# Performance work log

Measured on AMD Instinct MI355X. Metric: run time of the kernel, lower is better.

The kernel has to match this reference:

```python
import jax, jax.numpy as jnp
import numpy as np

N, C, E = 32768, 256, 16
LN_EPS = 1e-5
ENT_EPS = 1e-12


def setup_inputs() -> dict:
    key = jax.random.key(0)
    ks = jax.random.split(key, 8)
    return {
        "inputs": jax.random.normal(ks[0], (N, C), jnp.float32),
        "conv_out": jax.random.normal(ks[1], (N, C), jnp.float32),
        "domain_emb": jax.random.normal(ks[2], (C,), jnp.float32),
        "share_W": jax.random.normal(ks[3], (C, C), jnp.float32) * 0.02,
        "share_b": jnp.zeros((C,), jnp.float32),
        "gate_W": jax.random.normal(ks[4], (C, E), jnp.float32) * 0.1,
        "gate_b": jnp.zeros((E,), jnp.float32),
        "expert_W": jax.random.normal(ks[5], (E, C, C), jnp.float32) * 0.02,
        "expert_b": jnp.zeros((E, C), jnp.float32),
        "ln_gamma": jnp.ones((C,), jnp.float32),
        "ln_beta": jnp.zeros((C,), jnp.float32),
    }


def reference(inputs, conv_out, domain_emb, share_W, share_b, gate_W, gate_b,
              expert_W, expert_b, ln_gamma, ln_beta):
    n_exp = gate_W.shape[-1]

    # shared expert
    share_out = inputs @ share_W + share_b                      # (N, C)

    # LayerNorm on (stand-in) sparse-conv features + domain embedding
    mu = conv_out.mean(-1, keepdims=True)
    var = conv_out.var(-1, keepdims=True)
    route = (conv_out - mu) / jnp.sqrt(var + LN_EPS) * ln_gamma + ln_beta
    route = route + domain_emb                                   # (N, C)

    # router (eval path: no noise)
    gate_logits = route @ gate_W + gate_b                        # (N, E)
    w = jax.nn.softmax(gate_logits.astype(jnp.float32), axis=-1).astype(inputs.dtype)

    # entropy -> dynamic k per token
    entropy = -jnp.sum(w * jnp.log(w + ENT_EPS), axis=-1)        # (N,)
    max_entropy = jnp.log(jnp.float32(n_exp))
    k = jnp.ceil(1.0 + entropy / max_entropy * (n_exp - 1)).astype(jnp.int32)
    k = jnp.clip(k, 1, n_exp)                                    # (N,)

    # dynamic top-k selection mask (sort descending, keep first k)
    order = jnp.argsort(-w, axis=-1)                             # (N, E) descending ranks
    positions = jnp.arange(n_exp)[None, :]
    mask_sorted = positions < k[:, None]                         # (N, E) bool
    inv = jnp.argsort(order, axis=-1)                            # inverse permutation
    sel_mask = jnp.take_along_axis(mask_sorted, inv, axis=-1)    # (N, E) bool, expert-order
    combine = jnp.where(sel_mask, w, jnp.zeros_like(w))          # (N, E) combine weights

    # Switch-style load balancing loss
    frac_tokens = sel_mask.astype(jnp.float32).mean(0)           # (E,)
    frac_probs = w.astype(jnp.float32).mean(0)                   # (E,)
    loss_balance = jnp.mean(frac_tokens * frac_probs) * (n_exp ** 2)

    # expert compute + combine (dense, equivalent to gather/scatter loop)
    expert_out = jnp.einsum('nc,ecd->ned', inputs, expert_W) + expert_b  # (N, E, C)
    moe_out = jnp.einsum('ne,nec->nc', combine, expert_out)     # (N, C)

    return moe_out + share_out, loss_balance
```

## Files before the change

kernel.cpp:

```cpp
#include <hip/hip_runtime.h>
#include <hip/hip_bf16.h>

#define NTOK 32768
#define CH   256
#define NEXP 16

typedef __attribute__((ext_vector_type(8)))  short short8;
typedef __attribute__((ext_vector_type(16))) float f32x16;

#define MFMA32(a, b, c) __builtin_amdgcn_mfma_f32_32x32x16_bf16((a), (b), (c), 0, 0, 0)
#define BC8(v) __builtin_bit_cast(short8, (v))

static __device__ __forceinline__ unsigned short f2bf(float f) {
  unsigned int u = __builtin_bit_cast(unsigned int, f);
  unsigned int r = (u + 0x7fffu + ((u >> 16) & 1u)) >> 16;
  return (unsigned short)r;
}


__global__ __launch_bounds__(512, 2) void prep_kernel(
    const float* __restrict__ conv_out, const float* __restrict__ domain_emb,
    const float* __restrict__ gate_W, const float* __restrict__ gate_b,
    const float* __restrict__ ln_gamma, const float* __restrict__ ln_beta,
    const float* __restrict__ share_W, const float* __restrict__ expert_W,
    float* __restrict__ combine, float* __restrict__ frac_part,
    uint4* __restrict__ wp) {
  int t = threadIdx.x, b = blockIdx.x;

  if (b >= 512) {
    int g = (b - 512) * 512 + t;
    int e = g >> 13;
    int r = g & 8191;
    int lane = r & 63;
    int kb = (r >> 6) & 15;
    int db = r >> 10;
    int d  = db * 32 + (lane & 31);
    int k0 = kb * 16 + ((lane >> 5) << 3);
    const float* src = (e < 16) ? (expert_W + (size_t)e * 65536) : share_W;
    unsigned int p[4];
#pragma unroll
    for (int j = 0; j < 4; j++) {
      float f0 = src[(size_t)(k0 + 2 * j) * 256 + d];
      float f1 = src[(size_t)(k0 + 2 * j + 1) * 256 + d];
      p[j] = (unsigned int)f2bf(f0) | ((unsigned int)f2bf(f1) << 16);
    }
    wp[g] = make_uint4(p[0], p[1], p[2], p[3]);
    return;
  }

  __shared__ float route[8][256];
  __shared__ __align__(16) float gwT[16 * 260];
  __shared__ float fred[2][8][16];
  int w = t >> 6, l = t & 63;

#pragma unroll
  for (int i = 0; i < 8; i++) {
    int idx = i * 512 + t;
    gwT[(idx & 15) * 260 + (idx >> 4)] = gate_W[idx];
  }
  __syncthreads();

  int lc = l * 4;
  float4 g4 = *(const float4*)(ln_gamma + lc);
  float4 be4 = *(const float4*)(ln_beta + lc);
  float4 de4 = *(const float4*)(domain_emb + lc);
  int e = l & 15, q = l >> 4;
  float gb = gate_b[e];

  float4 gwreg[16];
#pragma unroll
  for (int ii = 0; ii < 16; ii++)
    gwreg[ii] = *(const float4*)&gwT[e * 260 + q * 64 + ii * 4];

  float psel = 0.f, pw = 0.f;
  int n0 = b * 64 + w * 8;
  float4 x = *(const float4*)(conv_out + (size_t)n0 * 256 + lc);
  for (int i = 0; i < 8; i++) {
    float4 xn = *(const float4*)(conv_out + (size_t)(n0 + ((i + 1) & 7)) * 256 + lc);

    float s1 = x.x + x.y + x.z + x.w;
#pragma unroll
    for (int off = 1; off < 64; off <<= 1) s1 += __shfl_xor(s1, off);
    float mu = s1 * (1.f / 256.f);
    float dx = x.x - mu, dy = x.y - mu, dz = x.z - mu, dw = x.w - mu;
    float s2 = dx * dx + dy * dy + dz * dz + dw * dw;
#pragma unroll
    for (int off = 1; off < 64; off <<= 1) s2 += __shfl_xor(s2, off);
    float rstd = rsqrtf(s2 * (1.f / 256.f) + 1e-5f);
    float4 r;
    r.x = dx * rstd * g4.x + be4.x + de4.x;
    r.y = dy * rstd * g4.y + be4.y + de4.y;
    r.z = dz * rstd * g4.z + be4.z + de4.z;
    r.w = dw * rstd * g4.w + be4.w + de4.w;
    *(float4*)(&route[w][lc]) = r;
    asm volatile("s_waitcnt lgkmcnt(0)" ::: "memory");
    __builtin_amdgcn_wave_barrier();

    float a0 = 0.f, a1 = 0.f, a2 = 0.f, a3 = 0.f;
#pragma unroll
    for (int ii = 0; ii < 16; ii += 4) {
      float4 r0 = *(const float4*)(&route[w][q * 64 + (ii + 0) * 4]);
      float4 r1 = *(const float4*)(&route[w][q * 64 + (ii + 1) * 4]);
      float4 r2 = *(const float4*)(&route[w][q * 64 + (ii + 2) * 4]);
      float4 r3 = *(const float4*)(&route[w][q * 64 + (ii + 3) * 4]);
      a0 += r0.x * gwreg[ii + 0].x + r0.y * gwreg[ii + 0].y + r0.z * gwreg[ii + 0].z + r0.w * gwreg[ii + 0].w;
      a1 += r1.x * gwreg[ii + 1].x + r1.y * gwreg[ii + 1].y + r1.z * gwreg[ii + 1].z + r1.w * gwreg[ii + 1].w;
      a2 += r2.x * gwreg[ii + 2].x + r2.y * gwreg[ii + 2].y + r2.z * gwreg[ii + 2].z + r2.w * gwreg[ii + 2].w;
      a3 += r3.x * gwreg[ii + 3].x + r3.y * gwreg[ii + 3].y + r3.z * gwreg[ii + 3].z + r3.w * gwreg[ii + 3].w;
    }
    float acc = (a0 + a1) + (a2 + a3);
    acc += __shfl_xor(acc, 16);
    acc += __shfl_xor(acc, 32);
    float logit = acc + gb;

    float m = logit;
#pragma unroll
    for (int off = 1; off < 16; off <<= 1) m = fmaxf(m, __shfl_xor(m, off));
    float p = expf(logit - m);
    float sum = p;
#pragma unroll
    for (int off = 1; off < 16; off <<= 1) sum += __shfl_xor(sum, off);
    float wv = p / sum;

    float et = -wv * logf(wv + 1e-12f);
    float ent = et;
#pragma unroll
    for (int off = 1; off < 16; off <<= 1) ent += __shfl_xor(ent, off);
    float kf = ceilf(1.f + ent * (15.f / 2.7725887f));
    int k = (int)kf;
    k = max(1, min(16, k));

    int base = l & 48;
    int rank = 0;
#pragma unroll
    for (int j = 0; j < 16; j++) {
      float wj = __shfl(wv, base + j);
      rank += (wj > wv) || (wj == wv && j < e);
    }
    int sel = rank < k;
    float cmb = sel ? wv : 0.f;
    int n = n0 + i;
    if (l < 16) combine[(size_t)n * 16 + e] = cmb;
    psel += (float)sel;
    pw += wv;

    x = xn;
  }

  if (l < 16) { fred[0][w][l] = psel; fred[1][w][l] = pw; }
  __syncthreads();
  if (t < 32) {
    int kind = t >> 4, ee = t & 15;
    float v = 0.f;
#pragma unroll
    for (int ww = 0; ww < 8; ww++) v += fred[kind][ww][ee];
    frac_part[b * 32 + t] = v;
  }
}

static __device__ __forceinline__ void pref_b4(
    uint4 (&breg)[4], const uint4* __restrict__ we, int q) {
#pragma unroll
  for (int kbl = 0; kbl < 4; kbl++) breg[kbl] = we[(q * 4 + kbl) * 64];
}

static __device__ __forceinline__ void slot_mfma4(
    f32x16 (&tacc)[2], const uint4* __restrict__ at, const uint4 (&breg)[4],
    int q, int hi, int r5) {
  __builtin_amdgcn_s_setprio(1);
#pragma unroll
  for (int kbl = 0; kbl < 4; kbl++) {
    int kb = q * 4 + kbl;
    int ax = kb * 128 + hi * 32 + (r5 ^ kb);
    short8 a0 = BC8(at[ax]);
    short8 a1 = BC8(at[ax + 64]);
    short8 bb = BC8(breg[kbl]);
    tacc[0] = MFMA32(a0, bb, tacc[0]);
    tacc[1] = MFMA32(a1, bb, tacc[1]);
  }
  __builtin_amdgcn_s_setprio(0);
}

__global__ __launch_bounds__(512, 4) void moe_gemm_kernel(
    const float* __restrict__ inputs, const uint4* __restrict__ wpack,
    const float* __restrict__ combine, const float* __restrict__ expert_b,
    const float* __restrict__ share_b, float* __restrict__ out,
    const float* __restrict__ frac_part) {
  extern __shared__ __align__(16) char smem[];
  int t = threadIdx.x, b = blockIdx.x;

  if (b == 512) {
    float* acc = (float*)smem;
    int col = t & 31, seg = t >> 5;
    float s = 0.f;
    for (int i = seg; i < 512; i += 16) s += frac_part[i * 32 + col];
    acc[seg * 32 + col] = s;
    __syncthreads();
    if (t < 32) {
      float v = 0.f;
#pragma unroll
      for (int sg = 0; sg < 16; sg++) v += acc[sg * 32 + t];
      acc[t] = v;
    }
    __syncthreads();
    if (t == 0) {
      float loss = 0.f;
      for (int e = 0; e < 16; e++) {
        float ft = acc[e] * (1.f / 32768.f);
        float fp = acc[16 + e] * (1.f / 32768.f);
        loss += ft * fp;
      }
      out[8388608] = loss * 16.f;
    }
    return;
  }

  uint4* at    = (uint4*)smem;
  float* wtile = (float*)(smem + 32768);

  int w = t >> 6, l = t & 63;
  int r5 = l & 31, hi = l >> 5;

#pragma unroll
  for (int i = 0; i < 4; i++) {
    int idx = i * 512 + t;
    int row = idx >> 5;
    int j = idx & 31;
    const float4* src = (const float4*)(inputs + ((size_t)b * 64 + row) * 256 + j * 8);
    float4 f0 = src[0], f1 = src[1];
    unsigned int p0 = (unsigned int)f2bf(f0.x) | ((unsigned int)f2bf(f0.y) << 16);
    unsigned int p1 = (unsigned int)f2bf(f0.z) | ((unsigned int)f2bf(f0.w) << 16);
    unsigned int p2 = (unsigned int)f2bf(f1.x) | ((unsigned int)f2bf(f1.y) << 16);
    unsigned int p3 = (unsigned int)f2bf(f1.z) | ((unsigned int)f2bf(f1.w) << 16);
    int kb = j >> 1, hib = j & 1;
    at[kb * 128 + (row >> 5) * 64 + hib * 32 + ((row & 31) ^ kb)] =
        make_uint4(p0, p1, p2, p3);
  }
  {
    const float* cg = combine + (size_t)b * 1024;
#pragma unroll
    for (int i = 0; i < 2; i++) {
      int idx = i * 512 + t;
      wtile[(idx & 15) * 64 + (idx >> 4)] = cg[idx];
    }
  }

  const uint4* wb = wpack + (size_t)w * 1024 + l;
  uint4 bregA[4], bregB[4];
  pref_b4(bregA, wb, 0);

  __syncthreads();

  f32x16 facc[2];
#pragma unroll
  for (int mb = 0; mb < 2; mb++)
#pragma unroll
    for (int r = 0; r < 16; r++) facc[mb][r] = 0.f;
  f32x16 tacc[2];
  int rowoff = hi * 4;

  for (int e = 0; e < 17; e++) {
    const uint4* we = wb + (size_t)e * 8192;
#pragma unroll
    for (int mb = 0; mb < 2; mb++)
#pragma unroll
      for (int r = 0; r < 16; r++) tacc[mb][r] = 0.f;

    pref_b4(bregB, we, 1);
    slot_mfma4(tacc, at, bregA, 0, hi, r5);
    pref_b4(bregA, we, 2);
    slot_mfma4(tacc, at, bregB, 1, hi, r5);
    pref_b4(bregB, we, 3);
    slot_mfma4(tacc, at, bregA, 2, hi, r5);
    if (e < 16) pref_b4(bregA, we + 8192, 0);
    slot_mfma4(tacc, at, bregB, 3, hi, r5);

    if (e < 16) {
#pragma unroll
      for (int mb = 0; mb < 2; mb++)
#pragma unroll
        for (int rg = 0; rg < 4; rg++) {
          float4 w4 = *(const float4*)&wtile[e * 64 + mb * 32 + 8 * rg + rowoff];
          float wj[4] = {w4.x, w4.y, w4.z, w4.w};
#pragma unroll
          for (int j = 0; j < 4; j++)
            facc[mb][rg * 4 + j] += wj[j] * tacc[mb][rg * 4 + j];
        }
    } else {
#pragma unroll
      for (int mb = 0; mb < 2; mb++)
#pragma unroll
        for (int r = 0; r < 16; r++) facc[mb][r] += tacc[mb][r];
    }
  }

  int col = w * 32 + r5;
  float sb = share_b[col];
  float eb[16];
#pragma unroll
  for (int e2 = 0; e2 < 16; e2++) eb[e2] = expert_b[e2 * 256 + col];
#pragma unroll
  for (int e2 = 0; e2 < 16; e2++)
#pragma unroll
    for (int mb = 0; mb < 2; mb++)
#pragma unroll
      for (int rg = 0; rg < 4; rg++) {
        float4 w4 = *(const float4*)&wtile[e2 * 64 + mb * 32 + 8 * rg + rowoff];
        float wj[4] = {w4.x, w4.y, w4.z, w4.w};
#pragma unroll
        for (int j = 0; j < 4; j++)
          facc[mb][rg * 4 + j] += wj[j] * eb[e2];
      }
#pragma unroll
  for (int mb = 0; mb < 2; mb++)
#pragma unroll
    for (int r = 0; r < 16; r++) {
      int row = mb * 32 + (r & 3) + ((r >> 2) << 3) + rowoff;
      out[((size_t)b * 64 + row) * 256 + col] = facc[mb][r] + sb;
    }
}

extern "C" void kernel_launch(void* const* d_in, const int* in_sizes, int n_in,
                              void* d_out, int out_size, void* d_ws, size_t ws_size,
                              hipStream_t stream) {
  const float* inputs   = (const float*)d_in[0];
  const float* conv_out = (const float*)d_in[1];
  const float* demb     = (const float*)d_in[2];
  const float* share_W  = (const float*)d_in[3];
  const float* share_b  = (const float*)d_in[4];
  const float* gate_W   = (const float*)d_in[5];
  const float* gate_b   = (const float*)d_in[6];
  const float* expert_W = (const float*)d_in[7];
  const float* expert_b = (const float*)d_in[8];
  const float* ln_g     = (const float*)d_in[9];
  const float* ln_b     = (const float*)d_in[10];
  float* out = (float*)d_out;
  char* ws = (char*)d_ws;

  uint4* wpack   = (uint4*)(ws);
  float* combine = (float*)(ws + 2228224);
  float* frac    = (float*)(ws + 4325376);

  hipFuncSetAttribute((const void*)moe_gemm_kernel,
                      hipFuncAttributeMaxDynamicSharedMemorySize, 36864);

  prep_kernel<<<dim3(784), dim3(512), 0, stream>>>(
      conv_out, demb, gate_W, gate_b, ln_g, ln_b, share_W, expert_W,
      combine, frac, wpack);
  moe_gemm_kernel<<<dim3(513), dim3(512), 36864, stream>>>(
      inputs, wpack, combine, expert_b, share_b, out, frac);
}
```

Measured before the change: 220.8 us.

## Pre-pack bf16 activations in prep kernel and hold A fragments in registers

Activation bf16 conversion and swizzled packing move from the GEMM kernel into extra blocks of the prep kernel, which write a packed buffer to the workspace. The GEMM kernel then loads its whole A tile into registers instead of LDS. Warps are re-split into 2 row groups by 4 column pairs, so each A fragment feeds two MFMAs against two B column blocks. This removes the per-block LDS staging and conversion from the GEMM. In exchange it adds a global round trip for the packed activations, raises register pressure, and lowers occupancy from 4 to 2 blocks per CU.

Result: slower. 245.0 us (+11.0%).

```diff
diff --git a/kernel.cpp b/kernel.cpp
--- a/kernel.cpp
+++ b/kernel.cpp
@@ -19,13 +19,42 @@
 
 
 __global__ __launch_bounds__(512, 2) void prep_kernel(
-    const float* __restrict__ conv_out, const float* __restrict__ domain_emb,
-    const float* __restrict__ gate_W, const float* __restrict__ gate_b,
-    const float* __restrict__ ln_gamma, const float* __restrict__ ln_beta,
-    const float* __restrict__ share_W, const float* __restrict__ expert_W,
-    float* __restrict__ combine, float* __restrict__ frac_part,
-    uint4* __restrict__ wp) {
+    const float* __restrict__ inputs, const float* __restrict__ conv_out,
+    const float* __restrict__ domain_emb, const float* __restrict__ gate_W,
+    const float* __restrict__ gate_b, const float* __restrict__ ln_gamma,
+    const float* __restrict__ ln_beta, const float* __restrict__ share_W,
+    const float* __restrict__ expert_W, float* __restrict__ combine,
+    float* __restrict__ frac_part, uint4* __restrict__ wp,
+    uint4* __restrict__ apack) {
+  __shared__ __align__(16) char shm[33280];
   int t = threadIdx.x, b = blockIdx.x;
+
+  if (b >= 784) {
+    uint4* at = (uint4*)shm;
+    int tile = b - 784;
+#pragma unroll
+    for (int i = 0; i < 4; i++) {
+      int u = i * 512 + t;
+      int row = u >> 5, j = u & 31;
+      const float4* src = (const float4*)(inputs + ((size_t)tile * 64 + row) * 256 + j * 8);
+      float4 f0 = src[0], f1 = src[1];
+      unsigned int p0 = (unsigned int)f2bf(f0.x) | ((unsigned int)f2bf(f0.y) << 16);
+      unsigned int p1 = (unsigned int)f2bf(f0.z) | ((unsigned int)f2bf(f0.w) << 16);
+      unsigned int p2 = (unsigned int)f2bf(f1.x) | ((unsigned int)f2bf(f1.y) << 16);
+      unsigned int p3 = (unsigned int)f2bf(f1.z) | ((unsigned int)f2bf(f1.w) << 16);
+      int kb = j >> 1, hib = j & 1;
+      at[kb * 128 + (row >> 5) * 64 + hib * 32 + ((row & 31) ^ kb)] =
+          make_uint4(p0, p1, p2, p3);
+    }
+    __syncthreads();
+#pragma unroll
+    for (int i = 0; i < 4; i++) {
+      int u = i * 512 + t;
+      int kb = u >> 7, mb = (u >> 6) & 1, hib = (u >> 5) & 1, r5 = u & 31;
+      apack[(size_t)tile * 2048 + u] = at[kb * 128 + mb * 64 + hib * 32 + (r5 ^ kb)];
+    }
+    return;
+  }
 
   if (b >= 512) {
     int g = (b - 512) * 512 + t;
@@ -48,9 +77,9 @@
     return;
   }
 
-  __shared__ float route[8][256];
-  __shared__ __align__(16) float gwT[16 * 260];
-  __shared__ float fred[2][8][16];
+  float (*route)[256] = (float(*)[256])shm;
+  float* gwT = (float*)(shm + 8192);
+  float* fred = (float*)(shm + 8192 + 16640);
   int w = t >> 6, l = t & 63;
 
 #pragma unroll
@@ -147,50 +176,50 @@
     x = xn;
   }
 
-  if (l < 16) { fred[0][w][l] = psel; fred[1][w][l] = pw; }
+  if (l < 16) { fred[0 * 128 + w * 16 + l] = psel; fred[1 * 128 + w * 16 + l] = pw; }
   __syncthreads();
   if (t < 32) {
     int kind = t >> 4, ee = t & 15;
     float v = 0.f;
 #pragma unroll
-    for (int ww = 0; ww < 8; ww++) v += fred[kind][ww][ee];
+    for (int ww = 0; ww < 8; ww++) v += fred[kind * 128 + ww * 16 + ee];
     frac_part[b * 32 + t] = v;
   }
 }
 
-static __device__ __forceinline__ void pref_b4(
-    uint4 (&breg)[4], const uint4* __restrict__ we, int q) {
-#pragma unroll
-  for (int kbl = 0; kbl < 4; kbl++) breg[kbl] = we[(q * 4 + kbl) * 64];
-}
-
-static __device__ __forceinline__ void slot_mfma4(
-    f32x16 (&tacc)[2], const uint4* __restrict__ at, const uint4 (&breg)[4],
-    int q, int hi, int r5) {
+static __device__ __forceinline__ void pref_b8(
+    uint4 (&breg)[8], const uint4* __restrict__ we, int qn) {
+#pragma unroll
+  for (int f = 0; f < 8; f++) {
+    int kbl = f >> 1, d = f & 1;
+    breg[f] = we[(size_t)d * 1024 + (qn * 4 + kbl) * 64];
+  }
+}
+
+static __device__ __forceinline__ void mfma8(
+    f32x16 (&tacc)[2], const uint4 (&areg)[16], const uint4 (&breg)[8], int q) {
   __builtin_amdgcn_s_setprio(1);
 #pragma unroll
   for (int kbl = 0; kbl < 4; kbl++) {
-    int kb = q * 4 + kbl;
-    int ax = kb * 128 + hi * 32 + (r5 ^ kb);
-    short8 a0 = BC8(at[ax]);
-    short8 a1 = BC8(at[ax + 64]);
-    short8 bb = BC8(breg[kbl]);
-    tacc[0] = MFMA32(a0, bb, tacc[0]);
-    tacc[1] = MFMA32(a1, bb, tacc[1]);
+    short8 a  = BC8(areg[q * 4 + kbl]);
+    short8 b0 = BC8(breg[kbl * 2 + 0]);
+    short8 b1 = BC8(breg[kbl * 2 + 1]);
+    tacc[0] = MFMA32(a, b0, tacc[0]);
+    tacc[1] = MFMA32(a, b1, tacc[1]);
   }
   __builtin_amdgcn_s_setprio(0);
 }
 
-__global__ __launch_bounds__(512, 4) void moe_gemm_kernel(
-    const float* __restrict__ inputs, const uint4* __restrict__ wpack,
+__global__ __launch_bounds__(512, 2) void moe_gemm_kernel(
+    const uint4* __restrict__ apack, const uint4* __restrict__ wpack,
     const float* __restrict__ combine, const float* __restrict__ expert_b,
     const float* __restrict__ share_b, float* __restrict__ out,
     const float* __restrict__ frac_part) {
-  extern __shared__ __align__(16) char smem[];
+  __shared__ __align__(16) float wtile[1024];
   int t = threadIdx.x, b = blockIdx.x;
 
   if (b == 512) {
-    float* acc = (float*)smem;
+    float* acc = wtile;
     int col = t & 31, seg = t >> 5;
     float s = 0.f;
     for (int i = seg; i < 512; i += 16) s += frac_part[i * 32 + col];
@@ -215,27 +244,11 @@
     return;
   }
 
-  uint4* at    = (uint4*)smem;
-  float* wtile = (float*)(smem + 32768);
-
   int w = t >> 6, l = t & 63;
+  int mw = w >> 2;
+  int dw = w & 3;
   int r5 = l & 31, hi = l >> 5;
 
-#pragma unroll
-  for (int i = 0; i < 4; i++) {
-    int idx = i * 512 + t;
-    int row = idx >> 5;
-    int j = idx & 31;
-    const float4* src = (const float4*)(inputs + ((size_t)b * 64 + row) * 256 + j * 8);
-    float4 f0 = src[0], f1 = src[1];
-    unsigned int p0 = (unsigned int)f2bf(f0.x) | ((unsigned int)f2bf(f0.y) << 16);
-    unsigned int p1 = (unsigned int)f2bf(f0.z) | ((unsigned int)f2bf(f0.w) << 16);
-    unsigned int p2 = (unsigned int)f2bf(f1.x) | ((unsigned int)f2bf(f1.y) << 16);
-    unsigned int p3 = (unsigned int)f2bf(f1.z) | ((unsigned int)f2bf(f1.w) << 16);
-    int kb = j >> 1, hib = j & 1;
-    at[kb * 128 + (row >> 5) * 64 + hib * 32 + ((row & 31) ^ kb)] =
-        make_uint4(p0, p1, p2, p3);
-  }
   {
     const float* cg = combine + (size_t)b * 1024;
 #pragma unroll
@@ -245,79 +258,89 @@
     }
   }
 
-  const uint4* wb = wpack + (size_t)w * 1024 + l;
-  uint4 bregA[4], bregB[4];
-  pref_b4(bregA, wb, 0);
+  const uint4* ab = apack + (size_t)b * 2048 + mw * 64 + l;
+  uint4 areg[16];
+#pragma unroll
+  for (int kb = 0; kb < 16; kb++) areg[kb] = ab[kb * 128];
+
+  const uint4* wb = wpack + (size_t)(dw * 2) * 1024 + l;
+  uint4 bregA[8], bregB[8];
+  pref_b8(bregA, wb, 0);
 
   __syncthreads();
 
   f32x16 facc[2];
 #pragma unroll
-  for (int mb = 0; mb < 2; mb++)
-#pragma unroll
-    for (int r = 0; r < 16; r++) facc[mb][r] = 0.f;
+  for (int d = 0; d < 2; d++)
+#pragma unroll
+    for (int r = 0; r < 16; r++) facc[d][r] = 0.f;
   f32x16 tacc[2];
   int rowoff = hi * 4;
 
   for (int e = 0; e < 17; e++) {
     const uint4* we = wb + (size_t)e * 8192;
 #pragma unroll
-    for (int mb = 0; mb < 2; mb++)
-#pragma unroll
-      for (int r = 0; r < 16; r++) tacc[mb][r] = 0.f;
-
-    pref_b4(bregB, we, 1);
-    slot_mfma4(tacc, at, bregA, 0, hi, r5);
-    pref_b4(bregA, we, 2);
-    slot_mfma4(tacc, at, bregB, 1, hi, r5);
-    pref_b4(bregB, we, 3);
-    slot_mfma4(tacc, at, bregA, 2, hi, r5);
-    if (e < 16) pref_b4(bregA, we + 8192, 0);
-    slot_mfma4(tacc, at, bregB, 3, hi, r5);
+    for (int d = 0; d < 2; d++)
+#pragma unroll
+      for (int r = 0; r < 16; r++) tacc[d][r] = 0.f;
+
+    pref_b8(bregB, we, 1);
+    mfma8(tacc, areg, bregA, 0);
+    pref_b8(bregA, we, 2);
+    mfma8(tacc, areg, bregB, 1);
+    pref_b8(bregB, we, 3);
+    mfma8(tacc, areg, bregA, 2);
+    if (e < 16) pref_b8(bregA, we + 8192, 0);
+    mfma8(tacc, areg, bregB, 3);
 
     if (e < 16) {
 #pragma unroll
-      for (int mb = 0; mb < 2; mb++)
-#pragma unroll
-        for (int rg = 0; rg < 4; rg++) {
-          float4 w4 = *(const float4*)&wtile[e * 64 + mb * 32 + 8 * rg + rowoff];
-          float wj[4] = {w4.x, w4.y, w4.z, w4.w};
-#pragma unroll
-          for (int j = 0; j < 4; j++)
-            facc[mb][rg * 4 + j] += wj[j] * tacc[mb][rg * 4 + j];
+      for (int rg = 0; rg < 4; rg++) {
+        float4 w4 = *(const float4*)&wtile[e * 64 + mw * 32 + 8 * rg + rowoff];
+        float wj[4] = {w4.x, w4.y, w4.z, w4.w};
+#pragma unroll
+        for (int j = 0; j < 4; j++) {
+          facc[0][rg * 4 + j] += wj[j] * tacc[0][rg * 4 + j];
+          facc[1][rg * 4 + j] += wj[j] * tacc[1][rg * 4 + j];
         }
+      }
     } else {
 #pragma unroll
-      for (int mb = 0; mb < 2; mb++)
-#pragma unroll
-        for (int r = 0; r < 16; r++) facc[mb][r] += tacc[mb][r];
-    }
-  }
-
-  int col = w * 32 + r5;
-  float sb = share_b[col];
-  float eb[16];
-#pragma unroll
-  for (int e2 = 0; e2 < 16; e2++) eb[e2] = expert_b[e2 * 256 + col];
+      for (int r = 0; r < 16; r++) {
+        facc[0][r] += tacc[0][r];
+        facc[1][r] += tacc[1][r];
+      }
+    }
+  }
+
+  int cg0 = (dw * 2 + 0) * 32 + r5;
+  int cg1 = (dw * 2 + 1) * 32 + r5;
+  float sb0 = share_b[cg0], sb1 = share_b[cg1];
+  float eb0[16], eb1[16];
+#pragma unroll
+  for (int e2 = 0; e2 < 16; e2++) {
+    eb0[e2] = expert_b[e2 * 256 + cg0];
+    eb1[e2] = expert_b[e2 * 256 + cg1];
+  }
 #pragma unroll
   for (int e2 = 0; e2 < 16; e2++)
 #pragma unroll
-    for (int mb = 0; mb < 2; mb++)
-#pragma unroll
-      for (int rg = 0; rg < 4; rg++) {
-        float4 w4 = *(const float4*)&wtile[e2 * 64 + mb * 32 + 8 * rg + rowoff];
-        float wj[4] = {w4.x, w4.y, w4.z, w4.w};
-#pragma unroll
-        for (int j = 0; j < 4; j++)
-          facc[mb][rg * 4 + j] += wj[j] * eb[e2];
+    for (int rg = 0; rg < 4; rg++) {
+      float4 w4 = *(const float4*)&wtile[e2 * 64 + mw * 32 + 8 * rg + rowoff];
+      float wj[4] = {w4.x, w4.y, w4.z, w4.w};
+#pragma unroll
+      for (int j = 0; j < 4; j++) {
+        facc[0][rg * 4 + j] += wj[j] * eb0[e2];
+        facc[1][rg * 4 + j] += wj[j] * eb1[e2];
       }
-#pragma unroll
-  for (int mb = 0; mb < 2; mb++)
-#pragma unroll
-    for (int r = 0; r < 16; r++) {
-      int row = mb * 32 + (r & 3) + ((r >> 2) << 3) + rowoff;
-      out[((size_t)b * 64 + row) * 256 + col] = facc[mb][r] + sb;
-    }
+    }
+#pragma unroll
+  for (int r = 0; r < 16; r++) {
+    int row = mw * 32 + (r & 3) + ((r >> 2) << 3) + rowoff;
+    size_t n = (size_t)b * 64 + row;
+    out[n * 256 + cg0] = facc[0][r] + sb0;
+    out[n * 256 + cg1] = facc[1][r] + sb1;
+  }
 }
 
 extern "C" void kernel_launch(void* const* d_in, const int* in_sizes, int n_in,
@@ -338,15 +361,13 @@
   char* ws = (char*)d_ws;
 
   uint4* wpack   = (uint4*)(ws);
-  float* combine = (float*)(ws + 2228224);
-  float* frac    = (float*)(ws + 4325376);
-
-  hipFuncSetAttribute((const void*)moe_gemm_kernel,
-                      hipFuncAttributeMaxDynamicSharedMemorySize, 36864);
-
-  prep_kernel<<<dim3(784), dim3(512), 0, stream>>>(
-      conv_out, demb, gate_W, gate_b, ln_g, ln_b, share_W, expert_W,
-      combine, frac, wpack);
-  moe_gemm_kernel<<<dim3(513), dim3(512), 36864, stream>>>(
-      inputs, wpack, combine, expert_b, share_b, out, frac);
-}
+  uint4* apack   = (uint4*)(ws + 2228224);
+  float* combine = (float*)(ws + 19005440);
+  float* frac    = (float*)(ws + 21102592);
+
+  prep_kernel<<<dim3(1296), dim3(512), 0, stream>>>(
+      inputs, conv_out, demb, gate_W, gate_b, ln_g, ln_b, share_W, expert_W,
+      combine, frac, wpack, apack);
+  moe_gemm_kernel<<<dim3(513), dim3(512), 0, stream>>>(
+      apack, wpack, combine, expert_b, share_b, out, frac);
+}
```
